# Kernel tuning notes

Measured on AMD Instinct MI355X. Metric: run time of the kernel, lower is better.

Reference implementation:

```python
import jax, jax.numpy as jnp
import numpy as np

N = 50000      # nodes
E = 800000     # edges (avg degree 16)
IN, H, OUT = 128, 256, 2
BN_EPS = 1e-5


def setup_inputs() -> dict:
    key = jax.random.key(0)
    ks = jax.random.split(key, 24)
    w = lambda k, s: jax.random.normal(k, s, jnp.float32) * 0.05
    inp = {
        "x": jax.random.normal(ks[0], (N, IN), jnp.float32),
        "edge_index": jax.random.randint(ks[1], (2, E), 0, N, jnp.int64),
    }
    # GINConv 1 MLP: Linear(IN,H) -> BN(H) -> ReLU -> Linear(H,H) -> ReLU
    inp.update(c1_W1=w(ks[2], (IN, H)), c1_b1=w(ks[3], (H,)),
               c1_g=jnp.ones((H,), jnp.float32), c1_be=jnp.zeros((H,), jnp.float32),
               c1_W2=w(ks[4], (H, H)), c1_b2=w(ks[5], (H,)))
    # GINConv 2
    inp.update(c2_W1=w(ks[6], (H, H)), c2_b1=w(ks[7], (H,)),
               c2_g=jnp.ones((H,), jnp.float32), c2_be=jnp.zeros((H,), jnp.float32),
               c2_W2=w(ks[8], (H, H)), c2_b2=w(ks[9], (H,)))
    # GINConv 3
    inp.update(c3_W1=w(ks[10], (H, H)), c3_b1=w(ks[11], (H,)),
               c3_g=jnp.ones((H,), jnp.float32), c3_be=jnp.zeros((H,), jnp.float32),
               c3_W2=w(ks[12], (H, H)), c3_b2=w(ks[13], (H,)))
    # readout head
    inp.update(lin1_W=w(ks[14], (3 * H, 3 * H)), lin1_b=w(ks[15], (3 * H,)),
               lin2_W=w(ks[16], (3 * H, OUT)), lin2_b=w(ks[17], (OUT,)))
    return inp


def _gin_conv(x, src, dst, W1, b1, g, be, W2, b2):
    # sum-aggregate neighbor features: agg[i] = sum_{e: dst[e]==i} x[src[e]]
    agg = jax.ops.segment_sum(x[src], dst, num_segments=N)
    h = (x + agg) @ W1 + b1            # (1+eps)*x + agg, eps=0
    mu = h.mean(axis=0)
    var = h.var(axis=0)                # biased var, as torch BN training
    h = jax.nn.relu((h - mu) * jax.lax.rsqrt(var + BN_EPS) * g + be)
    return jax.nn.relu(h @ W2 + b2)


def reference(x, edge_index,
              c1_W1, c1_b1, c1_g, c1_be, c1_W2, c1_b2,
              c2_W1, c2_b1, c2_g, c2_be, c2_W2, c2_b2,
              c3_W1, c3_b1, c3_g, c3_be, c3_W2, c3_b2,
              lin1_W, lin1_b, lin2_W, lin2_b):
    src, dst = edge_index[0], edge_index[1]
    h1 = _gin_conv(x, src, dst, c1_W1, c1_b1, c1_g, c1_be, c1_W2, c1_b2)
    h2 = _gin_conv(h1, src, dst, c2_W1, c2_b1, c2_g, c2_be, c2_W2, c2_b2)
    h3 = _gin_conv(h2, src, dst, c3_W1, c3_b1, c3_g, c3_be, c3_W2, c3_b2)
    h = jnp.concatenate((h1, h2, h3), axis=1)        # [N, 3H]
    h = jax.nn.relu(h @ lin1_W + lin1_b)
    h = h @ lin2_W + lin2_b                          # [N, OUT]
    return h, jax.nn.softmax(h, axis=1)
```

## Files before the change

### kernel.cpp

```cpp
#include <hip/hip_runtime.h>
#include <hip/hip_bf16.h>


#define GIN_N_FEAT_IN 128
#define GIN_H 256
#define M_PAD_ROWS 50176

typedef short short8 __attribute__((ext_vector_type(8)));
typedef float f32x4 __attribute__((ext_vector_type(4)));

#define SCHED_FENCE() __builtin_amdgcn_sched_barrier(0)
#define RAW_BARRIER() __builtin_amdgcn_s_barrier()

__device__ inline ushort f32_to_bf16(float f) {
    union { float f; uint u; } x; x.f = f;
    uint r = x.u + 0x7fff + ((x.u >> 16) & 1);
    return (ushort)(r >> 16);
}
__device__ inline float bf16_to_f32(uint h) {
    union { uint u; float f; } x; x.u = h << 16;
    return x.f;
}
__device__ inline uint pack_bf16(float lo, float hi) {
    return (uint)f32_to_bf16(lo) | ((uint)f32_to_bf16(hi) << 16);
}

__device__ inline void gload_lds16(const ushort* g, ushort* l) {
    __builtin_amdgcn_global_load_lds(
        (const __attribute__((address_space(1))) void*)g,
        (__attribute__((address_space(3))) void*)l, 16, 0, 0);
}


__global__ void cvt_f32_bf16(const float* __restrict__ in, ushort* __restrict__ out, int npairs) {
    for (int i = blockIdx.x * blockDim.x + threadIdx.x; i < npairs; i += gridDim.x * blockDim.x) {
        float2 v = ((const float2*)in)[i];
        ((uint*)out)[i] = pack_bf16(v.x, v.y);
    }
}

struct WPrep {
    const float* src[7];
    ushort* dst[7];
    int R[7];
    int C[7];
};

__global__ void prep_weights(WPrep p) {
    int which = blockIdx.y;
    int R = p.R[which], C = p.C[which];
    int total = R * C;
    const float* src = p.src[which];
    ushort* dst = p.dst[which];
    for (int idx = blockIdx.x * blockDim.x + threadIdx.x; idx < total;
         idx += gridDim.x * blockDim.x) {
        int r = idx / C, c = idx - r * C;
        dst[(size_t)c * R + r] = f32_to_bf16(src[idx]);
    }
}


__global__ void count_kernel(const int* __restrict__ ei, int* __restrict__ deg, int E) {
    for (int e = blockIdx.x * blockDim.x + threadIdx.x; e < E; e += gridDim.x * blockDim.x) {
        atomicAdd(&deg[ei[E + e]], 1);
    }
}

__global__ void scan_chunk(const int* __restrict__ deg, int* __restrict__ row_start,
                           int* __restrict__ chunk_sums, int N) {
    __shared__ int sm[256];
    int tid = threadIdx.x;
    int idx = blockIdx.x * 256 + tid;
    int v = (idx < N) ? deg[idx] : 0;
    sm[tid] = v;
    __syncthreads();
    #pragma unroll
    for (int off = 1; off < 256; off <<= 1) {
        int t = (tid >= off) ? sm[tid - off] : 0;
        __syncthreads();
        sm[tid] += t;
        __syncthreads();
    }
    if (idx < N) row_start[idx] = sm[tid] - v;
    if (tid == 255) chunk_sums[blockIdx.x] = sm[255];
}

__global__ void scan_tops(int* __restrict__ chunk_sums, int* __restrict__ row_start,
                          int nchunks, int N, int E) {
    __shared__ int sm[256];
    int tid = threadIdx.x;
    int v = (tid < nchunks) ? chunk_sums[tid] : 0;
    sm[tid] = v;
    __syncthreads();
    #pragma unroll
    for (int off = 1; off < 256; off <<= 1) {
        int t = (tid >= off) ? sm[tid - off] : 0;
        __syncthreads();
        sm[tid] += t;
        __syncthreads();
    }
    if (tid < nchunks) chunk_sums[tid] = sm[tid] - v;
    if (tid == 0) row_start[N] = E;
}

__global__ void scan_add(int* __restrict__ row_start, int* __restrict__ cursor,
                         const int* __restrict__ chunk_sums, int N) {
    int idx = blockIdx.x * 256 + threadIdx.x;
    if (idx < N) {
        int v = row_start[idx] + chunk_sums[blockIdx.x];
        row_start[idx] = v;
        cursor[idx] = v;
    }
}

__global__ void scatter_kernel(const int* __restrict__ ei, int* __restrict__ cursor,
                               int* __restrict__ perm, int E) {
    for (int e = blockIdx.x * blockDim.x + threadIdx.x; e < E; e += gridDim.x * blockDim.x) {
        int d = ei[E + e];
        int pos = atomicAdd(&cursor[d], 1);
        perm[pos] = ei[e];
    }
}


template <int W>
__global__ void agg2(const ushort* __restrict__ xsrc, int stride,
                     const int* __restrict__ row_start, const int* __restrict__ perm,
                     ushort* __restrict__ out, int N) {
    constexpr int PL = W / 64;
    int node = blockIdx.x * 4 + (threadIdx.x >> 6);
    if (node >= N) return;
    const int lane = threadIdx.x & 63;
    const size_t loff = (size_t)lane * PL;

    float af[PL];
    {
        const ushort* p = xsrc + (size_t)node * stride + loff;
        if constexpr (W == 256) {
            uint2 v = *(const uint2*)p;
            af[0] = bf16_to_f32(v.x & 0xffffu); af[1] = bf16_to_f32(v.x >> 16);
            af[2] = bf16_to_f32(v.y & 0xffffu); af[3] = bf16_to_f32(v.y >> 16);
        } else {
            uint v = *(const uint*)p;
            af[0] = bf16_to_f32(v & 0xffffu); af[1] = bf16_to_f32(v >> 16);
        }
    }
    const int s = row_start[node], e = row_start[node + 1];
    int j = s;
    for (; j + 4 <= e; j += 4) {
        int n0 = perm[j], n1 = perm[j + 1], n2 = perm[j + 2], n3 = perm[j + 3];
        if constexpr (W == 256) {
            uint2 w0 = *(const uint2*)(xsrc + (size_t)n0 * stride + loff);
            uint2 w1 = *(const uint2*)(xsrc + (size_t)n1 * stride + loff);
            uint2 w2 = *(const uint2*)(xsrc + (size_t)n2 * stride + loff);
            uint2 w3 = *(const uint2*)(xsrc + (size_t)n3 * stride + loff);
            af[0] += bf16_to_f32(w0.x & 0xffffu) + bf16_to_f32(w1.x & 0xffffu)
                   + bf16_to_f32(w2.x & 0xffffu) + bf16_to_f32(w3.x & 0xffffu);
            af[1] += bf16_to_f32(w0.x >> 16) + bf16_to_f32(w1.x >> 16)
                   + bf16_to_f32(w2.x >> 16) + bf16_to_f32(w3.x >> 16);
            af[2] += bf16_to_f32(w0.y & 0xffffu) + bf16_to_f32(w1.y & 0xffffu)
                   + bf16_to_f32(w2.y & 0xffffu) + bf16_to_f32(w3.y & 0xffffu);
            af[3] += bf16_to_f32(w0.y >> 16) + bf16_to_f32(w1.y >> 16)
                   + bf16_to_f32(w2.y >> 16) + bf16_to_f32(w3.y >> 16);
        } else {
            uint w0 = *(const uint*)(xsrc + (size_t)n0 * stride + loff);
            uint w1 = *(const uint*)(xsrc + (size_t)n1 * stride + loff);
            uint w2 = *(const uint*)(xsrc + (size_t)n2 * stride + loff);
            uint w3 = *(const uint*)(xsrc + (size_t)n3 * stride + loff);
            af[0] += bf16_to_f32(w0 & 0xffffu) + bf16_to_f32(w1 & 0xffffu)
                   + bf16_to_f32(w2 & 0xffffu) + bf16_to_f32(w3 & 0xffffu);
            af[1] += bf16_to_f32(w0 >> 16) + bf16_to_f32(w1 >> 16)
                   + bf16_to_f32(w2 >> 16) + bf16_to_f32(w3 >> 16);
        }
    }
    for (; j < e; ++j) {
        int sn = perm[j];
        const ushort* p = xsrc + (size_t)sn * stride + loff;
        if constexpr (W == 256) {
            uint2 w = *(const uint2*)p;
            af[0] += bf16_to_f32(w.x & 0xffffu); af[1] += bf16_to_f32(w.x >> 16);
            af[2] += bf16_to_f32(w.y & 0xffffu); af[3] += bf16_to_f32(w.y >> 16);
        } else {
            uint w = *(const uint*)p;
            af[0] += bf16_to_f32(w & 0xffffu); af[1] += bf16_to_f32(w >> 16);
        }
    }
    ushort* po = out + (size_t)node * W + loff;
    if constexpr (W == 256) {
        uint2 o; o.x = pack_bf16(af[0], af[1]); o.y = pack_bf16(af[2], af[3]);
        *(uint2*)po = o;
    } else {
        *(uint*)po = pack_bf16(af[0], af[1]);
    }
}


template <int MODE>
__global__ __launch_bounds__(256) void gemm_mfma(
    const ushort* __restrict__ A, const ushort* __restrict__ Bt,
    const float* __restrict__ bias, void* __restrict__ Cout,
    int ldc, int K, float* __restrict__ extra, int Nvalid) {
    __shared__ ushort As[3][128 * 32];
    __shared__ ushort Bs[3][128 * 32];
    const int tid = threadIdx.x;

    const int gx = gridDim.x;
    const int nwg = gx * gridDim.y;
    const int flat = blockIdx.y * gx + blockIdx.x;
    const int q = nwg >> 3, r = nwg & 7;
    const int xcd = flat & 7, loc = flat >> 3;
    const int wg = (xcd < r ? xcd * (q + 1) : r * (q + 1) + (xcd - r) * q) + loc;
    const int bm = (wg / gx) * 128;
    const int bn = (wg % gx) * 128;

    const int lane = tid & 63;
    const int wid = tid >> 6;
    const int wr = wid >> 1, wc = wid & 1;

    f32x4 acc[4][4] = {};

    const int arow = tid >> 2;
    const int gcol = ((tid & 3) ^ ((tid >> 3) & 3)) * 8;
    const ushort* Ag0 = A + (size_t)(bm + arow) * K + gcol;
    const ushort* Ag1 = A + (size_t)(bm + 64 + arow) * K + gcol;
    const ushort* Bg0 = Bt + (size_t)(bn + arow) * K + gcol;
    const ushort* Bg1 = Bt + (size_t)(bn + 64 + arow) * K + gcol;
    const int wofs = (tid & ~63) * 8;

    const int fr = lane & 15;
    const int rchunk = ((lane >> 4) ^ ((fr >> 1) & 3)) * 8;

    const int NT = K >> 5;

    #pragma unroll
    for (int t = 0; t < 2; ++t) {
        const int k0 = t << 5;
        ushort* a = As[t]; ushort* b = Bs[t];
        gload_lds16(Ag0 + k0, a + wofs);
        gload_lds16(Ag1 + k0, a + 2048 + wofs);
        gload_lds16(Bg0 + k0, b + wofs);
        gload_lds16(Bg1 + k0, b + 2048 + wofs);
    }

    int sl = 0;
    for (int it = 0; it < NT; ++it) {
        if (it + 2 < NT) {
            int wsl = sl + 2; if (wsl >= 3) wsl -= 3;
            const int k0 = (it + 2) << 5;
            ushort* a = As[wsl]; ushort* b = Bs[wsl];
            gload_lds16(Ag0 + k0, a + wofs);
            gload_lds16(Ag1 + k0, a + 2048 + wofs);
            gload_lds16(Bg0 + k0, b + wofs);
            gload_lds16(Bg1 + k0, b + 2048 + wofs);
            asm volatile("s_waitcnt vmcnt(8)" ::: "memory");
        } else if (it + 1 < NT) {
            asm volatile("s_waitcnt vmcnt(4)" ::: "memory");
        } else {
            asm volatile("s_waitcnt vmcnt(0)" ::: "memory");
        }
        SCHED_FENCE();
        RAW_BARRIER();

        const ushort* as = As[sl];
        const ushort* bs = Bs[sl];
        short8 af[4], bf[4];
        #pragma unroll
        for (int m = 0; m < 4; ++m)
            af[m] = *(const short8*)&as[(wr * 64 + m * 16 + fr) * 32 + rchunk];
        #pragma unroll
        for (int n = 0; n < 4; ++n)
            bf[n] = *(const short8*)&bs[(wc * 64 + n * 16 + fr) * 32 + rchunk];
        __builtin_amdgcn_s_setprio(1);
        #pragma unroll
        for (int m = 0; m < 4; ++m)
            #pragma unroll
            for (int n = 0; n < 4; ++n)
                acc[m][n] = __builtin_amdgcn_mfma_f32_16x16x32_bf16(af[m], bf[n], acc[m][n], 0, 0, 0);
        __builtin_amdgcn_s_setprio(0);

        asm volatile("s_waitcnt lgkmcnt(0)" ::: "memory");
        SCHED_FENCE();
        RAW_BARRIER();
        sl = sl + 1; if (sl >= 3) sl -= 3;
    }

    float s1[4], s2[4];
    if constexpr (MODE == 0) {
        #pragma unroll
        for (int n = 0; n < 4; ++n) { s1[n] = 0.f; s2[n] = 0.f; }
    }
    #pragma unroll
    for (int n = 0; n < 4; ++n) {
        const int col = bn + wc * 64 + n * 16 + fr;
        const float bv = bias[col];
        #pragma unroll
        for (int m = 0; m < 4; ++m) {
            const int row0 = bm + wr * 64 + m * 16 + (lane >> 4) * 4;
            #pragma unroll
            for (int rr = 0; rr < 4; ++rr) {
                float v = acc[m][n][rr] + bv;
                if constexpr (MODE == 1) {
                    v = fmaxf(v, 0.f);
                    ((ushort*)Cout)[(size_t)(row0 + rr) * ldc + col] = f32_to_bf16(v);
                } else {
                    ((float*)Cout)[(size_t)(row0 + rr) * ldc + col] = v;
                    if (row0 + rr < Nvalid) { s1[n] += v; s2[n] += v * v; }
                }
            }
        }
    }
    if constexpr (MODE == 0) {
        #pragma unroll
        for (int n = 0; n < 4; ++n) {
            float a = s1[n], b = s2[n];
            a += __shfl_xor(a, 16); b += __shfl_xor(b, 16);
            a += __shfl_xor(a, 32); b += __shfl_xor(b, 32);
            if ((lane >> 4) == 0) {
                int col = bn + wc * 64 + n * 16 + fr;
                atomicAdd(&extra[col], a);
                atomicAdd(&extra[256 + col], b);
            }
        }
    }
}


__global__ __launch_bounds__(512) void gemm_head(
    const ushort* __restrict__ A,
    const ushort* __restrict__ Bt,
    const float* __restrict__ bias,
    const float* __restrict__ w2,
    float* __restrict__ part,
    int K, int MP) {
    __shared__ ushort As[3][256 * 32];
    __shared__ ushort Bs[3][128 * 32];
    __shared__ float sm_part[256][2];
    const int tid = threadIdx.x;

    const int gx = gridDim.x;
    const int nwg = gx * gridDim.y;
    const int flat = blockIdx.y * gx + blockIdx.x;
    const int q = nwg >> 3, r = nwg & 7;
    const int xcd = flat & 7, loc = flat >> 3;
    const int wg = (xcd < r ? xcd * (q + 1) : r * (q + 1) + (xcd - r) * q) + loc;
    const int bm = (wg / gx) * 256;
    const int bn = (wg % gx) * 128;
    const int coltile = wg % gx;

    const int lane = tid & 63;
    const int wid = tid >> 6;
    const int wr = wid >> 1;
    const int wc = wid & 1;

    sm_part[tid >> 1][tid & 1] = 0.f;

    f32x4 acc[4][4] = {};

    const int arow = tid >> 2;
    const int gcol = ((tid & 3) ^ ((tid >> 3) & 3)) * 8;
    const ushort* Ag0 = A + (size_t)(bm + arow) * K + gcol;
    const ushort* Ag1 = A + (size_t)(bm + 128 + arow) * K + gcol;
    const ushort* Bg0 = Bt + (size_t)(bn + arow) * K + gcol;
    const int wofs = (tid & ~63) * 8;

    const int fr = lane & 15;
    const int rchunk = ((lane >> 4) ^ ((fr >> 1) & 3)) * 8;

    const int NT = K >> 5;

    #pragma unroll
    for (int t = 0; t < 2; ++t) {
        const int k0 = t << 5;
        ushort* a = As[t]; ushort* b = Bs[t];
        gload_lds16(Ag0 + k0, a + wofs);
        gload_lds16(Ag1 + k0, a + 4096 + wofs);
        gload_lds16(Bg0 + k0, b + wofs);
    }

    int sl = 0;
    for (int it = 0; it < NT; ++it) {
        if (it + 2 < NT) {
            int wsl = sl + 2; if (wsl >= 3) wsl -= 3;
            const int k0 = (it + 2) << 5;
            ushort* a = As[wsl]; ushort* b = Bs[wsl];
            gload_lds16(Ag0 + k0, a + wofs);
            gload_lds16(Ag1 + k0, a + 4096 + wofs);
            gload_lds16(Bg0 + k0, b + wofs);
            asm volatile("s_waitcnt vmcnt(6)" ::: "memory");
        } else if (it + 1 < NT) {
            asm volatile("s_waitcnt vmcnt(3)" ::: "memory");
        } else {
            asm volatile("s_waitcnt vmcnt(0)" ::: "memory");
        }
        SCHED_FENCE();
        RAW_BARRIER();

        const ushort* as = As[sl];
        const ushort* bs = Bs[sl];
        short8 af[4], bf[4];
        #pragma unroll
        for (int m = 0; m < 4; ++m)
            af[m] = *(const short8*)&as[(wr * 64 + m * 16 + fr) * 32 + rchunk];
        #pragma unroll
        for (int n = 0; n < 4; ++n)
            bf[n] = *(const short8*)&bs[(wc * 64 + n * 16 + fr) * 32 + rchunk];
        __builtin_amdgcn_s_setprio(1);
        #pragma unroll
        for (int m = 0; m < 4; ++m)
            #pragma unroll
            for (int n = 0; n < 4; ++n)
                acc[m][n] = __builtin_amdgcn_mfma_f32_16x16x32_bf16(af[m], bf[n], acc[m][n], 0, 0, 0);
        __builtin_amdgcn_s_setprio(0);

        asm volatile("s_waitcnt lgkmcnt(0)" ::: "memory");
        SCHED_FENCE();
        RAW_BARRIER();
        sl = sl + 1; if (sl >= 3) sl -= 3;
    }

    #pragma unroll
    for (int m = 0; m < 4; ++m) {
        #pragma unroll
        for (int rr = 0; rr < 4; ++rr) {
            float o0 = 0.f, o1 = 0.f;
            #pragma unroll
            for (int n = 0; n < 4; ++n) {
                int col = bn + wc * 64 + n * 16 + fr;
                float v = fmaxf(acc[m][n][rr] + bias[col], 0.f);
                o0 = fmaf(v, w2[col * 2 + 0], o0);
                o1 = fmaf(v, w2[col * 2 + 1], o1);
            }
            o0 += __shfl_xor(o0, 1); o1 += __shfl_xor(o1, 1);
            o0 += __shfl_xor(o0, 2); o1 += __shfl_xor(o1, 2);
            o0 += __shfl_xor(o0, 4); o1 += __shfl_xor(o1, 4);
            o0 += __shfl_xor(o0, 8); o1 += __shfl_xor(o1, 8);
            if (fr == 0) {
                int lrow = wr * 64 + m * 16 + (lane >> 4) * 4 + rr;
                atomicAdd(&sm_part[lrow][0], o0);
                atomicAdd(&sm_part[lrow][1], o1);
            }
        }
    }
    __syncthreads();
    {
        int lrow = tid >> 1, comp = tid & 1;
        part[((size_t)coltile * MP + bm + lrow) * 2 + comp] = sm_part[lrow][comp];
    }
}


__global__ void bn_apply(const float* __restrict__ h, const float* __restrict__ sums,
                         const float* __restrict__ g, const float* __restrict__ be,
                         ushort* __restrict__ outb, int Nrows) {
    int total = Nrows * 128;
    float inv = 1.0f / (float)Nrows;
    for (int idx = blockIdx.x * blockDim.x + threadIdx.x; idx < total;
         idx += gridDim.x * blockDim.x) {
        int row = idx >> 7;
        int cp = (idx & 127) * 2;
        float2 v = *(const float2*)(h + (size_t)row * 256 + cp);
        float mu0 = sums[cp] * inv,     mu1 = sums[cp + 1] * inv;
        float va0 = sums[256 + cp] * inv - mu0 * mu0;
        float va1 = sums[257 + cp] * inv - mu1 * mu1;
        float o0 = fmaxf((v.x - mu0) * rsqrtf(va0 + 1e-5f) * g[cp]     + be[cp],     0.f);
        float o1 = fmaxf((v.y - mu1) * rsqrtf(va1 + 1e-5f) * g[cp + 1] + be[cp + 1], 0.f);
        *(uint*)(outb + (size_t)row * 256 + cp) = pack_bf16(o0, o1);
    }
}


__global__ void finalize6(const float* __restrict__ part, const float* __restrict__ b2,
                          float* __restrict__ out, int Nrows, int MP) {
    int i = blockIdx.x * blockDim.x + threadIdx.x;
    if (i >= Nrows) return;
    float h0 = b2[0], h1 = b2[1];
    #pragma unroll
    for (int c = 0; c < 6; ++c) {
        h0 += part[((size_t)c * MP + i) * 2 + 0];
        h1 += part[((size_t)c * MP + i) * 2 + 1];
    }
    out[2 * i] = h0;
    out[2 * i + 1] = h1;
    float m = fmaxf(h0, h1);
    float e0 = expf(h0 - m), e1 = expf(h1 - m);
    float s = e0 + e1;
    out[(size_t)2 * Nrows + 2 * i] = e0 / s;
    out[(size_t)2 * Nrows + 2 * i + 1] = e1 / s;
}


extern "C" void kernel_launch(void* const* d_in, const int* in_sizes, int n_in,
                              void* d_out, int out_size, void* d_ws, size_t ws_size,
                              hipStream_t stream) {
    const int N = in_sizes[0] / GIN_N_FEAT_IN;
    const int E = in_sizes[1] / 2;
    const int MP = M_PAD_ROWS;
    const int nchunks = (N + 255) / 256;

    const float* x  = (const float*)d_in[0];
    const int*   ei = (const int*)d_in[1];
    const float* cW1[3] = {(const float*)d_in[2],  (const float*)d_in[8],  (const float*)d_in[14]};
    const float* cb1[3] = {(const float*)d_in[3],  (const float*)d_in[9],  (const float*)d_in[15]};
    const float* cg [3] = {(const float*)d_in[4],  (const float*)d_in[10], (const float*)d_in[16]};
    const float* cbe[3] = {(const float*)d_in[5],  (const float*)d_in[11], (const float*)d_in[17]};
    const float* cW2[3] = {(const float*)d_in[6],  (const float*)d_in[12], (const float*)d_in[18]};
    const float* cb2[3] = {(const float*)d_in[7],  (const float*)d_in[13], (const float*)d_in[19]};
    const float* lin1_W = (const float*)d_in[20];
    const float* lin1_b = (const float*)d_in[21];
    const float* lin2_W = (const float*)d_in[22];
    const float* lin2_b = (const float*)d_in[23];
    float* out = (float*)d_out;

    char* ws = (char*)d_ws;
    size_t off = 0;
    auto carve = [&](size_t bytes) {
        void* p = ws + off;
        off += (bytes + 255) & ~(size_t)255;
        return p;
    };
    ushort* Hcat   = (ushort*)carve((size_t)MP * 768 * 2);
    float*  hlin   = (float*) carve((size_t)MP * 256 * 4);
    ushort* hlin_b = (ushort*)carve((size_t)MP * 256 * 2);
    ushort* hpre   = (ushort*)carve((size_t)MP * 256 * 2);
    ushort* xb     = (ushort*)carve((size_t)MP * 128 * 2);
    ushort* w1t[3] = {(ushort*)carve(256 * 256 * 2), (ushort*)carve(256 * 256 * 2),
                      (ushort*)carve(256 * 256 * 2)};
    ushort* w2t[3] = {(ushort*)carve(256 * 256 * 2), (ushort*)carve(256 * 256 * 2),
                      (ushort*)carve(256 * 256 * 2)};
    ushort* lin1t  = (ushort*)carve((size_t)768 * 768 * 2);
    int*   row_st  = (int*)carve((size_t)(N + 1) * 4);
    int*   cursor  = (int*)carve((size_t)N * 4);
    int*   perm    = (int*)carve((size_t)E * 4);
    int*   csums   = (int*)carve(256 * 4);
    float* bnsums  = (float*)carve(512 * 4);
    float* part    = (float*)carve((size_t)6 * MP * 2 * 4);
    (void)ws_size;

    cvt_f32_bf16<<<1024, 256, 0, stream>>>(x, xb, N * 64);
    WPrep wp;
    wp.src[0] = cW1[0]; wp.dst[0] = w1t[0]; wp.R[0] = 128; wp.C[0] = 256;
    wp.src[1] = cW1[1]; wp.dst[1] = w1t[1]; wp.R[1] = 256; wp.C[1] = 256;
    wp.src[2] = cW1[2]; wp.dst[2] = w1t[2]; wp.R[2] = 256; wp.C[2] = 256;
    wp.src[3] = cW2[0]; wp.dst[3] = w2t[0]; wp.R[3] = 256; wp.C[3] = 256;
    wp.src[4] = cW2[1]; wp.dst[4] = w2t[1]; wp.R[4] = 256; wp.C[4] = 256;
    wp.src[5] = cW2[2]; wp.dst[5] = w2t[2]; wp.R[5] = 256; wp.C[5] = 256;
    wp.src[6] = lin1_W; wp.dst[6] = lin1t;  wp.R[6] = 768; wp.C[6] = 768;
    prep_weights<<<dim3(576, 7), 256, 0, stream>>>(wp);

    hipMemsetAsync(cursor, 0, (size_t)N * 4, stream);
    count_kernel<<<1024, 256, 0, stream>>>(ei, cursor, E);
    scan_chunk<<<nchunks, 256, 0, stream>>>(cursor, row_st, csums, N);
    scan_tops<<<1, 256, 0, stream>>>(csums, row_st, nchunks, N, E);
    scan_add<<<nchunks, 256, 0, stream>>>(row_st, cursor, csums, N);
    scatter_kernel<<<1024, 256, 0, stream>>>(ei, cursor, perm, E);

    const dim3 ggrid(2, MP / 128);
    const int aggblocks = (N + 3) / 4;

    for (int L = 0; L < 3; ++L) {
        if (L == 0)
            agg2<128><<<aggblocks, 256, 0, stream>>>(xb, 128, row_st, perm, hpre, N);
        else
            agg2<256><<<aggblocks, 256, 0, stream>>>(Hcat + (size_t)(L - 1) * 256, 768,
                                                     row_st, perm, hpre, N);

        hipMemsetAsync(bnsums, 0, 512 * 4, stream);
        gemm_mfma<0><<<ggrid, 256, 0, stream>>>(
            hpre, w1t[L], cb1[L], hlin, 256, (L == 0) ? 128 : 256, bnsums, N);

        bn_apply<<<2048, 256, 0, stream>>>(hlin, bnsums, cg[L], cbe[L], hlin_b, N);

        gemm_mfma<1><<<ggrid, 256, 0, stream>>>(
            hlin_b, w2t[L], cb2[L], (void*)(Hcat + (size_t)L * 256), 768, 256,
            nullptr, 0);
    }

    gemm_head<<<dim3(6, MP / 256), 512, 0, stream>>>(
        Hcat, lin1t, lin1_b, lin2_W, part, 768, MP);

    finalize6<<<(N + 255) / 256, 256, 0, stream>>>(part, lin2_b, out, N, MP);
}
```

Measured before the change: 671.5 us.

## Split 256-wide aggregation across two waves and restructure head GEMM pipeline

The 256-wide neighbor aggregation now uses two wavefronts per node, each covering 128 columns with 4-byte loads, which doubles the waves in flight for the gather. The head GEMM moves from a triple-buffered K=32 pipeline to a double-buffered K=64 tile with an 8-way XOR swizzle. Each iteration is split into two MFMA halves, with the next tile's global-to-LDS loads interleaved between them. This aims to raise memory-level parallelism and cut barriers per K, but it spends more LDS and waits on vmcnt(0) every iteration.

```diff
diff --git a/kernel.cpp b/kernel.cpp
--- a/kernel.cpp
+++ b/kernel.cpp
@@ -123,75 +123,76 @@
 }
 
 
-template <int W>
-__global__ void agg2(const ushort* __restrict__ xsrc, int stride,
-                     const int* __restrict__ row_start, const int* __restrict__ perm,
-                     ushort* __restrict__ out, int N) {
-    constexpr int PL = W / 64;
+__global__ void agg128(const ushort* __restrict__ xsrc,
+                       const int* __restrict__ row_start, const int* __restrict__ perm,
+                       ushort* __restrict__ out, int N) {
     int node = blockIdx.x * 4 + (threadIdx.x >> 6);
     if (node >= N) return;
     const int lane = threadIdx.x & 63;
-    const size_t loff = (size_t)lane * PL;
-
-    float af[PL];
+    const size_t loff = (size_t)lane * 2;
+    const ushort* base = xsrc + loff;
+
+    float lo, hi;
     {
-        const ushort* p = xsrc + (size_t)node * stride + loff;
-        if constexpr (W == 256) {
-            uint2 v = *(const uint2*)p;
-            af[0] = bf16_to_f32(v.x & 0xffffu); af[1] = bf16_to_f32(v.x >> 16);
-            af[2] = bf16_to_f32(v.y & 0xffffu); af[3] = bf16_to_f32(v.y >> 16);
-        } else {
-            uint v = *(const uint*)p;
-            af[0] = bf16_to_f32(v & 0xffffu); af[1] = bf16_to_f32(v >> 16);
-        }
+        uint v = *(const uint*)(base + (size_t)node * 128);
+        lo = bf16_to_f32(v & 0xffffu); hi = bf16_to_f32(v >> 16);
     }
     const int s = row_start[node], e = row_start[node + 1];
     int j = s;
     for (; j + 4 <= e; j += 4) {
         int n0 = perm[j], n1 = perm[j + 1], n2 = perm[j + 2], n3 = perm[j + 3];
-        if constexpr (W == 256) {
-            uint2 w0 = *(const uint2*)(xsrc + (size_t)n0 * stride + loff);
-            uint2 w1 = *(const uint2*)(xsrc + (size_t)n1 * stride + loff);
-            uint2 w2 = *(const uint2*)(xsrc + (size_t)n2 * stride + loff);
-            uint2 w3 = *(const uint2*)(xsrc + (size_t)n3 * stride + loff);
-            af[0] += bf16_to_f32(w0.x & 0xffffu) + bf16_to_f32(w1.x & 0xffffu)
-                   + bf16_to_f32(w2.x & 0xffffu) + bf16_to_f32(w3.x & 0xffffu);
-            af[1] += bf16_to_f32(w0.x >> 16) + bf16_to_f32(w1.x >> 16)
-                   + bf16_to_f32(w2.x >> 16) + bf16_to_f32(w3.x >> 16);
-            af[2] += bf16_to_f32(w0.y & 0xffffu) + bf16_to_f32(w1.y & 0xffffu)
-                   + bf16_to_f32(w2.y & 0xffffu) + bf16_to_f32(w3.y & 0xffffu);
-            af[3] += bf16_to_f32(w0.y >> 16) + bf16_to_f32(w1.y >> 16)
-                   + bf16_to_f32(w2.y >> 16) + bf16_to_f32(w3.y >> 16);
-        } else {
-            uint w0 = *(const uint*)(xsrc + (size_t)n0 * stride + loff);
-            uint w1 = *(const uint*)(xsrc + (size_t)n1 * stride + loff);
-            uint w2 = *(const uint*)(xsrc + (size_t)n2 * stride + loff);
-            uint w3 = *(const uint*)(xsrc + (size_t)n3 * stride + loff);
-            af[0] += bf16_to_f32(w0 & 0xffffu) + bf16_to_f32(w1 & 0xffffu)
-                   + bf16_to_f32(w2 & 0xffffu) + bf16_to_f32(w3 & 0xffffu);
-            af[1] += bf16_to_f32(w0 >> 16) + bf16_to_f32(w1 >> 16)
-                   + bf16_to_f32(w2 >> 16) + bf16_to_f32(w3 >> 16);
-        }
+        uint w0 = *(const uint*)(base + (size_t)n0 * 128);
+        uint w1 = *(const uint*)(base + (size_t)n1 * 128);
+        uint w2 = *(const uint*)(base + (size_t)n2 * 128);
+        uint w3 = *(const uint*)(base + (size_t)n3 * 128);
+        lo += bf16_to_f32(w0 & 0xffffu) + bf16_to_f32(w1 & 0xffffu)
+            + bf16_to_f32(w2 & 0xffffu) + bf16_to_f32(w3 & 0xffffu);
+        hi += bf16_to_f32(w0 >> 16) + bf16_to_f32(w1 >> 16)
+            + bf16_to_f32(w2 >> 16) + bf16_to_f32(w3 >> 16);
     }
     for (; j < e; ++j) {
-        int sn = perm[j];
-        const ushort* p = xsrc + (size_t)sn * stride + loff;
-        if constexpr (W == 256) {
-            uint2 w = *(const uint2*)p;
-            af[0] += bf16_to_f32(w.x & 0xffffu); af[1] += bf16_to_f32(w.x >> 16);
-            af[2] += bf16_to_f32(w.y & 0xffffu); af[3] += bf16_to_f32(w.y >> 16);
-        } else {
-            uint w = *(const uint*)p;
-            af[0] += bf16_to_f32(w & 0xffffu); af[1] += bf16_to_f32(w >> 16);
-        }
-    }
-    ushort* po = out + (size_t)node * W + loff;
-    if constexpr (W == 256) {
-        uint2 o; o.x = pack_bf16(af[0], af[1]); o.y = pack_bf16(af[2], af[3]);
-        *(uint2*)po = o;
-    } else {
-        *(uint*)po = pack_bf16(af[0], af[1]);
-    }
+        uint w = *(const uint*)(base + (size_t)perm[j] * 128);
+        lo += bf16_to_f32(w & 0xffffu);
+        hi += bf16_to_f32(w >> 16);
+    }
+    *(uint*)(out + (size_t)node * 128 + loff) = pack_bf16(lo, hi);
+}
+
+
+__global__ void agg256_split(const ushort* __restrict__ xsrc, int stride,
+                             const int* __restrict__ row_start, const int* __restrict__ perm,
+                             ushort* __restrict__ out, int N) {
+    const int wid = threadIdx.x >> 6;
+    const int node = blockIdx.x * 2 + (wid >> 1);
+    if (node >= N) return;
+    const int lane = threadIdx.x & 63;
+    const int col = (wid & 1) * 128 + lane * 2;
+    const ushort* base = xsrc + col;
+
+    float lo, hi;
+    {
+        uint v = *(const uint*)(base + (size_t)node * stride);
+        lo = bf16_to_f32(v & 0xffffu); hi = bf16_to_f32(v >> 16);
+    }
+    const int s = row_start[node], e = row_start[node + 1];
+    int j = s;
+    for (; j + 4 <= e; j += 4) {
+        int n0 = perm[j], n1 = perm[j + 1], n2 = perm[j + 2], n3 = perm[j + 3];
+        uint w0 = *(const uint*)(base + (size_t)n0 * stride);
+        uint w1 = *(const uint*)(base + (size_t)n1 * stride);
+        uint w2 = *(const uint*)(base + (size_t)n2 * stride);
+        uint w3 = *(const uint*)(base + (size_t)n3 * stride);
+        lo += bf16_to_f32(w0 & 0xffffu) + bf16_to_f32(w1 & 0xffffu)
+            + bf16_to_f32(w2 & 0xffffu) + bf16_to_f32(w3 & 0xffffu);
+        hi += bf16_to_f32(w0 >> 16) + bf16_to_f32(w1 >> 16)
+            + bf16_to_f32(w2 >> 16) + bf16_to_f32(w3 >> 16);
+    }
+    for (; j < e; ++j) {
+        uint w = *(const uint*)(base + (size_t)perm[j] * stride);
+        lo += bf16_to_f32(w & 0xffffu);
+        hi += bf16_to_f32(w >> 16);
+    }
+    *(uint*)(out + (size_t)node * 256 + col) = pack_bf16(lo, hi);
 }
 
 
@@ -332,8 +333,8 @@
     const float* __restrict__ w2,
     float* __restrict__ part,
     int K, int MP) {
-    __shared__ ushort As[3][256 * 32];
-    __shared__ ushort Bs[3][128 * 32];
+    __shared__ ushort As[2][256 * 64];
+    __shared__ ushort Bs[2][128 * 64];
     __shared__ float sm_part[256][2];
     const int tid = threadIdx.x;
 
@@ -356,66 +357,108 @@
 
     f32x4 acc[4][4] = {};
 
-    const int arow = tid >> 2;
-    const int gcol = ((tid & 3) ^ ((tid >> 3) & 3)) * 8;
-    const ushort* Ag0 = A + (size_t)(bm + arow) * K + gcol;
-    const ushort* Ag1 = A + (size_t)(bm + 128 + arow) * K + gcol;
-    const ushort* Bg0 = Bt + (size_t)(bn + arow) * K + gcol;
+    const int srow = tid >> 3;
+    const int sgc = ((tid & 7) ^ ((tid >> 3) & 7)) * 8;
+    const ushort* AgBase = A + (size_t)(bm + srow) * K + sgc;
+    const ushort* BgBase = Bt + (size_t)(bn + srow) * K + sgc;
+    const size_t rowK64 = (size_t)64 * K;
     const int wofs = (tid & ~63) * 8;
 
     const int fr = lane & 15;
-    const int rchunk = ((lane >> 4) ^ ((fr >> 1) & 3)) * 8;
-
-    const int NT = K >> 5;
-
-    #pragma unroll
-    for (int t = 0; t < 2; ++t) {
-        const int k0 = t << 5;
-        ushort* a = As[t]; ushort* b = Bs[t];
-        gload_lds16(Ag0 + k0, a + wofs);
-        gload_lds16(Ag1 + k0, a + 4096 + wofs);
-        gload_lds16(Bg0 + k0, b + wofs);
-    }
-
-    int sl = 0;
+    const int ch = lane >> 4;
+
+    const int NT = K >> 6;
+
+    {
+        ushort* a = As[0]; ushort* b = Bs[0];
+        gload_lds16(AgBase + 0 * rowK64, a + 0 * 4096 + wofs);
+        gload_lds16(AgBase + 1 * rowK64, a + 1 * 4096 + wofs);
+        gload_lds16(AgBase + 2 * rowK64, a + 2 * 4096 + wofs);
+        gload_lds16(AgBase + 3 * rowK64, a + 3 * 4096 + wofs);
+        gload_lds16(BgBase + 0 * rowK64, b + 0 * 4096 + wofs);
+        gload_lds16(BgBase + 1 * rowK64, b + 1 * 4096 + wofs);
+    }
+
     for (int it = 0; it < NT; ++it) {
-        if (it + 2 < NT) {
-            int wsl = sl + 2; if (wsl >= 3) wsl -= 3;
-            const int k0 = (it + 2) << 5;
-            ushort* a = As[wsl]; ushort* b = Bs[wsl];
-            gload_lds16(Ag0 + k0, a + wofs);
-            gload_lds16(Ag1 + k0, a + 4096 + wofs);
-            gload_lds16(Bg0 + k0, b + wofs);
-            asm volatile("s_waitcnt vmcnt(6)" ::: "memory");
-        } else if (it + 1 < NT) {
-            asm volatile("s_waitcnt vmcnt(3)" ::: "memory");
-        } else {
-            asm volatile("s_waitcnt vmcnt(0)" ::: "memory");
-        }
+        asm volatile("s_waitcnt vmcnt(0)" ::: "memory");
         SCHED_FENCE();
         RAW_BARRIER();
 
-        const ushort* as = As[sl];
-        const ushort* bs = Bs[sl];
-        short8 af[4], bf[4];
-        #pragma unroll
-        for (int m = 0; m < 4; ++m)
-            af[m] = *(const short8*)&as[(wr * 64 + m * 16 + fr) * 32 + rchunk];
-        #pragma unroll
-        for (int n = 0; n < 4; ++n)
-            bf[n] = *(const short8*)&bs[(wc * 64 + n * 16 + fr) * 32 + rchunk];
-        __builtin_amdgcn_s_setprio(1);
-        #pragma unroll
-        for (int m = 0; m < 4; ++m)
-            #pragma unroll
-            for (int n = 0; n < 4; ++n)
-                acc[m][n] = __builtin_amdgcn_mfma_f32_16x16x32_bf16(af[m], bf[n], acc[m][n], 0, 0, 0);
-        __builtin_amdgcn_s_setprio(0);
-
+        const ushort* as = As[it & 1];
+        const ushort* bs = Bs[it & 1];
+        ushort* an = As[(it + 1) & 1];
+        ushort* bnx = Bs[(it + 1) & 1];
+        const bool pf = (it + 1 < NT);
+        const int kg = (it + 1) << 6;
+
+        short8 bfr[4][2], afr[2][2];
+
+        #pragma unroll
+        for (int n = 0; n < 4; ++n) {
+            const int row = wc * 64 + n * 16 + fr;
+            #pragma unroll
+            for (int ks = 0; ks < 2; ++ks) {
+                const int c = ks * 4 + ch;
+                bfr[n][ks] = *(const short8*)&bs[row * 64 + ((c ^ (row & 7)) * 8)];
+            }
+        }
+        #pragma unroll
+        for (int m = 0; m < 2; ++m) {
+            const int row = wr * 64 + m * 16 + fr;
+            #pragma unroll
+            for (int ks = 0; ks < 2; ++ks) {
+                const int c = ks * 4 + ch;
+                afr[m][ks] = *(const short8*)&as[row * 64 + ((c ^ (row & 7)) * 8)];
+            }
+        }
+        if (pf) {
+            gload_lds16(AgBase + kg + 0 * rowK64, an + 0 * 4096 + wofs);
+            gload_lds16(AgBase + kg + 1 * rowK64, an + 1 * 4096 + wofs);
+            gload_lds16(AgBase + kg + 2 * rowK64, an + 2 * 4096 + wofs);
+        }
+        RAW_BARRIER();
         asm volatile("s_waitcnt lgkmcnt(0)" ::: "memory");
         SCHED_FENCE();
+        __builtin_amdgcn_s_setprio(1);
+        #pragma unroll
+        for (int m = 0; m < 2; ++m)
+            #pragma unroll
+            for (int ks = 0; ks < 2; ++ks)
+                #pragma unroll
+                for (int n = 0; n < 4; ++n)
+                    acc[m][n] = __builtin_amdgcn_mfma_f32_16x16x32_bf16(
+                        afr[m][ks], bfr[n][ks], acc[m][n], 0, 0, 0);
+        __builtin_amdgcn_s_setprio(0);
+        SCHED_FENCE();
         RAW_BARRIER();
-        sl = sl + 1; if (sl >= 3) sl -= 3;
+
+        #pragma unroll
+        for (int m = 0; m < 2; ++m) {
+            const int row = wr * 64 + (m + 2) * 16 + fr;
+            #pragma unroll
+            for (int ks = 0; ks < 2; ++ks) {
+                const int c = ks * 4 + ch;
+                afr[m][ks] = *(const short8*)&as[row * 64 + ((c ^ (row & 7)) * 8)];
+            }
+        }
+        if (pf) {
+            gload_lds16(AgBase + kg + 3 * rowK64, an + 3 * 4096 + wofs);
+            gload_lds16(BgBase + kg + 0 * rowK64, bnx + 0 * 4096 + wofs);
+            gload_lds16(BgBase + kg + 1 * rowK64, bnx + 1 * 4096 + wofs);
+        }
+        RAW_BARRIER();
+        asm volatile("s_waitcnt lgkmcnt(0)" ::: "memory");
+        SCHED_FENCE();
+        __builtin_amdgcn_s_setprio(1);
+        #pragma unroll
+        for (int m = 0; m < 2; ++m)
+            #pragma unroll
+            for (int ks = 0; ks < 2; ++ks)
+                #pragma unroll
+                for (int n = 0; n < 4; ++n)
+                    acc[m + 2][n] = __builtin_amdgcn_mfma_f32_16x16x32_bf16(
+                        afr[m][ks], bfr[n][ks], acc[m + 2][n], 0, 0, 0);
+        __builtin_amdgcn_s_setprio(0);
     }
 
     #pragma unroll
@@ -555,14 +598,13 @@
     scatter_kernel<<<1024, 256, 0, stream>>>(ei, cursor, perm, E);
 
     const dim3 ggrid(2, MP / 128);
-    const int aggblocks = (N + 3) / 4;
 
     for (int L = 0; L < 3; ++L) {
         if (L == 0)
-            agg2<128><<<aggblocks, 256, 0, stream>>>(xb, 128, row_st, perm, hpre, N);
+            agg128<<<(N + 3) / 4, 256, 0, stream>>>(xb, row_st, perm, hpre, N);
         else
-            agg2<256><<<aggblocks, 256, 0, stream>>>(Hcat + (size_t)(L - 1) * 256, 768,
-                                                     row_st, perm, hpre, N);
+            agg256_split<<<(N + 1) / 2, 256, 0, stream>>>(
+                Hcat + (size_t)(L - 1) * 256, 768, row_st, perm, hpre, N);
 
         hipMemsetAsync(bnsums, 0, 512 * 4, stream);
         gemm_mfma<0><<<ggrid, 256, 0, stream>>>(
```

Result: slower. 694.9 us (+3.5%).

## Enlarge head GEMM tile to 256x256 with BK=64 double buffering

Applied to the files above, without the earlier changes.

The readout head GEMM now uses 256x256 output tiles with a K-step of 64 and two LDS buffers instead of 256x128 tiles, K-step 32 and three buffers. Each wave computes a 128x64 sub-tile with 8x4 accumulators, and the LDS swizzle is switched to an 8-chunk XOR pattern. This halves the column tiles, so A is re-read from global memory half as often and finalize sums three partials instead of six. In exchange it uses more registers and LDS per block, has shallower pipelining, and launches half as many blocks.

```diff
diff --git a/kernel.cpp b/kernel.cpp
--- a/kernel.cpp
+++ b/kernel.cpp
@@ -332,8 +332,8 @@
     const float* __restrict__ w2,
     float* __restrict__ part,
     int K, int MP) {
-    __shared__ ushort As[3][256 * 32];
-    __shared__ ushort Bs[3][128 * 32];
+    __shared__ ushort As[2][256 * 64];
+    __shared__ ushort Bs[2][256 * 64];
     __shared__ float sm_part[256][2];
     const int tid = threadIdx.x;
 
@@ -344,82 +344,88 @@
     const int xcd = flat & 7, loc = flat >> 3;
     const int wg = (xcd < r ? xcd * (q + 1) : r * (q + 1) + (xcd - r) * q) + loc;
     const int bm = (wg / gx) * 256;
-    const int bn = (wg % gx) * 128;
+    const int bn = (wg % gx) * 256;
     const int coltile = wg % gx;
 
     const int lane = tid & 63;
     const int wid = tid >> 6;
-    const int wr = wid >> 1;
-    const int wc = wid & 1;
+    const int wr = wid >> 2;
+    const int wc = wid & 3;
 
     sm_part[tid >> 1][tid & 1] = 0.f;
 
-    f32x4 acc[4][4] = {};
-
-    const int arow = tid >> 2;
-    const int gcol = ((tid & 3) ^ ((tid >> 3) & 3)) * 8;
-    const ushort* Ag0 = A + (size_t)(bm + arow) * K + gcol;
-    const ushort* Ag1 = A + (size_t)(bm + 128 + arow) * K + gcol;
-    const ushort* Bg0 = Bt + (size_t)(bn + arow) * K + gcol;
+    f32x4 acc[8][4] = {};
+
+    const int srow = tid >> 3;
+    const int sgc = ((tid & 7) ^ ((tid >> 3) & 7)) * 8;
+    const ushort* AgBase = A + (size_t)(bm + srow) * K + sgc;
+    const ushort* BgBase = Bt + (size_t)(bn + srow) * K + sgc;
+    const size_t rowK64 = (size_t)64 * K;
     const int wofs = (tid & ~63) * 8;
 
     const int fr = lane & 15;
-    const int rchunk = ((lane >> 4) ^ ((fr >> 1) & 3)) * 8;
-
-    const int NT = K >> 5;
-
-    #pragma unroll
-    for (int t = 0; t < 2; ++t) {
-        const int k0 = t << 5;
-        ushort* a = As[t]; ushort* b = Bs[t];
-        gload_lds16(Ag0 + k0, a + wofs);
-        gload_lds16(Ag1 + k0, a + 4096 + wofs);
-        gload_lds16(Bg0 + k0, b + wofs);
-    }
-
-    int sl = 0;
+    const int ch = lane >> 4;
+
+    const int NT = K >> 6;
+
+    {
+        ushort* a = As[0]; ushort* b = Bs[0];
+        #pragma unroll
+        for (int p = 0; p < 4; ++p) {
+            gload_lds16(AgBase + p * rowK64, a + p * 4096 + wofs);
+            gload_lds16(BgBase + p * rowK64, b + p * 4096 + wofs);
+        }
+    }
+
     for (int it = 0; it < NT; ++it) {
-        if (it + 2 < NT) {
-            int wsl = sl + 2; if (wsl >= 3) wsl -= 3;
-            const int k0 = (it + 2) << 5;
-            ushort* a = As[wsl]; ushort* b = Bs[wsl];
-            gload_lds16(Ag0 + k0, a + wofs);
-            gload_lds16(Ag1 + k0, a + 4096 + wofs);
-            gload_lds16(Bg0 + k0, b + wofs);
-            asm volatile("s_waitcnt vmcnt(6)" ::: "memory");
-        } else if (it + 1 < NT) {
-            asm volatile("s_waitcnt vmcnt(3)" ::: "memory");
+        if (it + 1 < NT) {
+            const int kg = (it + 1) << 6;
+            ushort* a = As[(it + 1) & 1]; ushort* b = Bs[(it + 1) & 1];
+            #pragma unroll
+            for (int p = 0; p < 4; ++p) {
+                gload_lds16(AgBase + kg + p * rowK64, a + p * 4096 + wofs);
+                gload_lds16(BgBase + kg + p * rowK64, b + p * 4096 + wofs);
+            }
+            asm volatile("s_waitcnt vmcnt(8)" ::: "memory");
         } else {
             asm volatile("s_waitcnt vmcnt(0)" ::: "memory");
         }
         SCHED_FENCE();
         RAW_BARRIER();
 
-        const ushort* as = As[sl];
-        const ushort* bs = Bs[sl];
-        short8 af[4], bf[4];
-        #pragma unroll
-        for (int m = 0; m < 4; ++m)
-            af[m] = *(const short8*)&as[(wr * 64 + m * 16 + fr) * 32 + rchunk];
-        #pragma unroll
-        for (int n = 0; n < 4; ++n)
-            bf[n] = *(const short8*)&bs[(wc * 64 + n * 16 + fr) * 32 + rchunk];
-        __builtin_amdgcn_s_setprio(1);
-        #pragma unroll
-        for (int m = 0; m < 4; ++m)
-            #pragma unroll
-            for (int n = 0; n < 4; ++n)
-                acc[m][n] = __builtin_amdgcn_mfma_f32_16x16x32_bf16(af[m], bf[n], acc[m][n], 0, 0, 0);
-        __builtin_amdgcn_s_setprio(0);
+        const ushort* as = As[it & 1];
+        const ushort* bs = Bs[it & 1];
+        #pragma unroll
+        for (int ks = 0; ks < 2; ++ks) {
+            const int lc = ks * 4 + ch;
+            short8 afr[8], bfr[4];
+            #pragma unroll
+            for (int m = 0; m < 8; ++m) {
+                const int row = wr * 128 + m * 16 + fr;
+                afr[m] = *(const short8*)&as[row * 64 + ((lc ^ (row & 7)) * 8)];
+            }
+            #pragma unroll
+            for (int n = 0; n < 4; ++n) {
+                const int row = wc * 64 + n * 16 + fr;
+                bfr[n] = *(const short8*)&bs[row * 64 + ((lc ^ (row & 7)) * 8)];
+            }
+            __builtin_amdgcn_s_setprio(1);
+            #pragma unroll
+            for (int m = 0; m < 8; ++m)
+                #pragma unroll
+                for (int n = 0; n < 4; ++n)
+                    acc[m][n] = __builtin_amdgcn_mfma_f32_16x16x32_bf16(
+                        afr[m], bfr[n], acc[m][n], 0, 0, 0);
+            __builtin_amdgcn_s_setprio(0);
+        }
 
         asm volatile("s_waitcnt lgkmcnt(0)" ::: "memory");
         SCHED_FENCE();
         RAW_BARRIER();
-        sl = sl + 1; if (sl >= 3) sl -= 3;
     }
 
     #pragma unroll
-    for (int m = 0; m < 4; ++m) {
+    for (int m = 0; m < 8; ++m) {
         #pragma unroll
         for (int rr = 0; rr < 4; ++rr) {
             float o0 = 0.f, o1 = 0.f;
@@ -435,7 +441,7 @@
             o0 += __shfl_xor(o0, 4); o1 += __shfl_xor(o1, 4);
             o0 += __shfl_xor(o0, 8); o1 += __shfl_xor(o1, 8);
             if (fr == 0) {
-                int lrow = wr * 64 + m * 16 + (lane >> 4) * 4 + rr;
+                int lrow = wr * 128 + m * 16 + (lane >> 4) * 4 + rr;
                 atomicAdd(&sm_part[lrow][0], o0);
                 atomicAdd(&sm_part[lrow][1], o1);
             }
@@ -469,13 +475,13 @@
 }
 
 
-__global__ void finalize6(const float* __restrict__ part, const float* __restrict__ b2,
+__global__ void finalize3(const float* __restrict__ part, const float* __restrict__ b2,
                           float* __restrict__ out, int Nrows, int MP) {
     int i = blockIdx.x * blockDim.x + threadIdx.x;
     if (i >= Nrows) return;
     float h0 = b2[0], h1 = b2[1];
     #pragma unroll
-    for (int c = 0; c < 6; ++c) {
+    for (int c = 0; c < 3; ++c) {
         h0 += part[((size_t)c * MP + i) * 2 + 0];
         h1 += part[((size_t)c * MP + i) * 2 + 1];
     }
@@ -533,7 +539,7 @@
     int*   perm    = (int*)carve((size_t)E * 4);
     int*   csums   = (int*)carve(256 * 4);
     float* bnsums  = (float*)carve(512 * 4);
-    float* part    = (float*)carve((size_t)6 * MP * 2 * 4);
+    float* part    = (float*)carve((size_t)3 * MP * 2 * 4);
     (void)ws_size;
 
     cvt_f32_bf16<<<1024, 256, 0, stream>>>(x, xb, N * 64);
@@ -575,8 +581,8 @@
             nullptr, 0);
     }
 
-    gemm_head<<<dim3(6, MP / 256), 512, 0, stream>>>(
+    gemm_head<<<dim3(3, MP / 256), 512, 0, stream>>>(
         Hcat, lin1t, lin1_b, lin2_W, part, 768, MP);
 
-    finalize6<<<(N + 255) / 256, 256, 0, stream>>>(part, lin2_b, out, N, MP);
-}
+    finalize3<<<(N + 255) / 256, 256, 0, stream>>>(part, lin2_b, out, N, MP);
+}
```

After: 683.2 us. Within noise of the previous version (+1.7%).
